# Performance work log

Hardware: AMD Instinct MI355X
Metric: run time of the kernel (lower is better)

Reference implementation:

```python
import jax, jax.numpy as jnp
import numpy as np

WINDOWS = [2, 4, 6]
THR = 0.5


def conv1x1(x, w, b):
    # x: [N,C,H,W], w: [O,C], b: [O]
    return jnp.einsum('nchw,oc->nohw', x, w) + b[None, :, None, None]


def cpool(x):
    # channel max + mean -> [N,2,H,W]
    return jnp.stack([x.max(axis=1), x.mean(axis=1)], axis=1)


def mask_fusion(orin, feature, w1, b1, w2, b2):
    sim = jax.nn.sigmoid(jnp.sum(conv1x1(cpool(orin), w1, b1) * conv1x1(cpool(feature), w2, b2), axis=1, keepdims=True))
    mask = (sim > THR).astype(orin.dtype)
    return mask * feature + (1.0 - mask) * orin


def unfold(x, kh, kw, sh, sw, w):
    # torch F.unfold equivalent -> [N, C*kh*kw, w*w] (channel-major like torch)
    rows = jnp.arange(w)[:, None] * sh + jnp.arange(kh)[None, :]  # [w,kh]
    cols = jnp.arange(w)[:, None] * sw + jnp.arange(kw)[None, :]  # [w,kw]
    p = x[:, :, rows[:, :, None, None], cols[None, None, :, :]]  # [N,C,w,kh,w,kw]
    p = p.transpose(0, 1, 3, 5, 2, 4)  # [N,C,kh,kw,w,w]
    N, C = x.shape[:2]
    return p.reshape(N, C * kh * kw, w * w)


def fold(cols_, H, W, kh, kw, sh, sw, w):
    # torch F.fold equivalent (col2im with overlap-add)
    N, CK, P = cols_.shape
    C = CK // (kh * kw)
    p = cols_.reshape(N, C, kh, kw, w, w).transpose(0, 1, 4, 2, 5, 3).reshape(N, C, w * kh, w * kw)
    r = (jnp.arange(w)[:, None] * sh + jnp.arange(kh)[None, :]).reshape(-1)
    c = (jnp.arange(w)[:, None] * sw + jnp.arange(kw)[None, :]).reshape(-1)
    return jnp.zeros((N, C, H, W), cols_.dtype).at[:, :, r[:, None], c[None, :]].add(p)


def psa(u, wq, wk, wv):
    # u: [N,C,P,L]; scaled dot-product self-attention over L within each patch
    t = u.transpose(0, 2, 3, 1)  # [N,P,L,C]
    q, k, v = t @ wq, t @ wk, t @ wv
    s = jnp.einsum('nplc,npmc->nplm', q, k) / jnp.sqrt(jnp.asarray(t.shape[-1], t.dtype))
    o = jnp.einsum('nplm,npmc->nplc', jax.nn.softmax(s, axis=-1), v)
    return o.transpose(0, 3, 1, 2)


def setup_inputs():
    key = jax.random.key(0)
    ks = jax.random.split(key, 20)
    N, C, H, W = 4, 64, 72, 72
    E = len(WINDOWS) * C
    nrm = lambda k, shape, s: jax.random.normal(k, shape, jnp.float32) * s
    return {
        'x': nrm(ks[0], (N, C, H, W), 1.0),
        'exp_w': nrm(ks[1], (E, C), C ** -0.5), 'exp_b': jnp.zeros((E,), jnp.float32),
        'res_w': nrm(ks[2], (C, E), E ** -0.5), 'res_b': jnp.zeros((C,), jnp.float32),
        'fus_w': nrm(ks[3], (C, C), C ** -0.5), 'fus_b': jnp.zeros((C,), jnp.float32),
        'wq': nrm(ks[4], (C, C), C ** -0.5),
        'wk': nrm(ks[5], (C, C), C ** -0.5),
        'wv': nrm(ks[6], (C, C), C ** -0.5),
        'mf1a_w': nrm(ks[7], (2, 2), 0.7), 'mf1a_b': jnp.zeros((2,), jnp.float32),
        'mf1b_w': nrm(ks[8], (2, 2), 0.7), 'mf1b_b': jnp.zeros((2,), jnp.float32),
        'mf2a_w': nrm(ks[9], (2, 2), 0.7), 'mf2a_b': jnp.zeros((2,), jnp.float32),
        'mf2b_w': nrm(ks[10], (2, 2), 0.7), 'mf2b_b': jnp.zeros((2,), jnp.float32),
    }


def reference(x, exp_w, exp_b, res_w, res_b, fus_w, fus_b, wq, wk, wv,
              mf1a_w, mf1a_b, mf1b_w, mf1b_b, mf2a_w, mf2a_b, mf2b_w, mf2b_b):
    N, C, H, W = x.shape
    expx = conv1x1(x, exp_w, exp_b)  # [N, 3C, H, W]
    parts = jnp.split(expx, len(WINDOWS), axis=1)
    outs = []
    for i, w in enumerate(WINDOWS):
        sh, sw = H // w, W // w
        kh, kw = sh + H % w, sw + W % w
        u = unfold(parts[i], kh, kw, sh, sw, w)       # [N, C*kh*kw, w*w]
        u = u.reshape(N, C, w * w, kh * kw)           # raw reinterpret, as in torch .view
        a = psa(u, wq, wk, wv).reshape(N, C * kh * kw, w * w)
        cnt = fold(jnp.ones_like(a), H, W, kh, kw, sh, sw, w)
        outs.append(fold(a, H, W, kh, kw, sh, sw, w) / cnt)
    out = mask_fusion(jnp.concatenate(outs, axis=1), expx, mf1a_w, mf1a_b, mf1b_w, mf1b_b)
    out = conv1x1(out, res_w, res_b)
    out = mask_fusion(out, x, mf2a_w, mf2a_b, mf2b_w, mf2b_b)
    return conv1x1(out, fus_w, fus_b)
```

## Files before the change

kernel.cpp:

```cpp
#include <hip/hip_runtime.h>

constexpr int CN = 4;
constexpr int CC = 64;
constexpr int CH = 72, CW = 72;
constexpr int HW = CH * CW;
constexpr int NPOS = CN * HW;
constexpr long TOKF = 3L * NPOS * 64;
constexpr long HPAD = 4096;

typedef _Float16 h4 __attribute__((ext_vector_type(4)));
typedef _Float16 h8 __attribute__((ext_vector_type(8)));
typedef float f4 __attribute__((ext_vector_type(4)));

__device__ __forceinline__ int fidx(int row, int g, int off) {
  return (row << 6) + ((g ^ (row & 7)) << 3) + off;
}
__device__ __forceinline__ int f192(int row, int g) {
  return row * 192 + (((g & 24) | ((g ^ row) & 7)) << 3);
}

template <int WW, int SS>
__device__ __forceinline__ void expand_body(const float* __restrict__ x,
                                            const float* __restrict__ w64,
                                            const float* __restrict__ b64,
                                            float* __restrict__ out, int pg) {
  int n = pg / HW;
  int pos = pg - n * HW;
  int h = pos / CW, wcol = pos % CW;

  float xv[64];
  const float* xp = x + (long)n * CC * HW + pos;
#pragma unroll
  for (int c = 0; c < 64; ++c) xv[c] = xp[c * HW];

  int wr = h / SS, kx = h % SS, wcq = wcol / SS, ky = wcol % SS;
  int j = kx * (SS * WW * WW) + ky * (WW * WW) + wr * WW + wcq;
  float* op = out + ((long)n * HW + j) * 64;

#pragma unroll 1
  for (int og = 0; og < 16; ++og) {
    float t0[4];
#pragma unroll
    for (int i = 0; i < 4; ++i) {
      int o = og * 4 + i;
      float acc = b64[o];
      const float* wp = w64 + o * 64;
#pragma unroll
      for (int cg = 0; cg < 16; ++cg) {
        float4 w4 = *(const float4*)(wp + 4 * cg);
        acc = fmaf(xv[4 * cg + 0], w4.x, acc);
        acc = fmaf(xv[4 * cg + 1], w4.y, acc);
        acc = fmaf(xv[4 * cg + 2], w4.z, acc);
        acc = fmaf(xv[4 * cg + 3], w4.w, acc);
      }
      t0[i] = acc;
    }
    *(float4*)(op + og * 4) = make_float4(t0[0], t0[1], t0[2], t0[3]);
  }
}

__global__ __launch_bounds__(256) void k_prep(
    const float* __restrict__ x, const float* __restrict__ exp_w,
    const float* __restrict__ exp_b, const float* __restrict__ wq,
    const float* __restrict__ wk, const float* __restrict__ wv,
    const float* __restrict__ res_w, const float* __restrict__ fus_w,
    float* __restrict__ ex, _Float16* __restrict__ wTh,
    _Float16* __restrict__ wTl, _Float16* __restrict__ rwh,
    _Float16* __restrict__ rwl, _Float16* __restrict__ fwh,
    _Float16* __restrict__ fwl) {
  int b = blockIdx.x;
  if (b >= 243) {
    int i = (b - 243) * 256 + threadIdx.x;
    float v;
    _Float16 *dh, *dl;
    int off;
    if (i < 12288) {
      int m = i >> 12;
      int r = i & 4095;
      int cp = r >> 6, c = r & 63;
      const float* src = (m == 0) ? wq : ((m == 1) ? wk : wv);
      v = src[c * 64 + cp];
      dh = wTh; dl = wTl; off = i;
    } else if (i < 24576) {
      off = i - 12288;
      v = res_w[off];
      dh = rwh; dl = rwl;
    } else {
      off = i - 24576;
      v = fus_w[off];
      dh = fwh; dl = fwl;
    }
    _Float16 h = (_Float16)v;
    dh[off] = h;
    dl[off] = (_Float16)(v - (float)h);
    return;
  }
  int wi = b / 81;
  int pg = (b - wi * 81) * 256 + threadIdx.x;
  if (wi == 0)
    expand_body<2, 36>(x, exp_w, exp_b, ex, pg);
  else if (wi == 1)
    expand_body<4, 18>(x, exp_w + 4096, exp_b + 64, ex + (long)NPOS * 64, pg);
  else
    expand_body<6, 12>(x, exp_w + 8192, exp_b + 128, ex + 2L * NPOS * 64, pg);
}

__global__ __launch_bounds__(256) void k_qkv(
    const float* __restrict__ ex, const _Float16* __restrict__ wTh,
    const _Float16* __restrict__ wTl, _Float16* __restrict__ qh,
    _Float16* __restrict__ ql, _Float16* __restrict__ kh,
    _Float16* __restrict__ kl, _Float16* __restrict__ vth,
    _Float16* __restrict__ vtl) {
  __shared__ __align__(16) _Float16 Wh[12288], Wl[12288];
  __shared__ __align__(16) float Cb[4096];
  _Float16* Eh = (_Float16*)Cb;
  _Float16* El = (_Float16*)Cb + 4096;

  const int tid = threadIdx.x;
  const long tok0 = (long)blockIdx.x * 64;
  const int lane = tid & 63, w = tid >> 6;
  const int lw = lane & 15, lg = lane >> 4;

  {
    int srow = tid >> 2, sfq = tid & 3;
#pragma unroll
    for (int p = 0; p < 4; ++p) {
      int c0 = (4 * p + sfq) * 4;
      float4 v = *(const float4*)(ex + (tok0 + srow) * 64 + c0);
      h4 hh = {(_Float16)v.x, (_Float16)v.y, (_Float16)v.z, (_Float16)v.w};
      h4 ll = {(_Float16)(v.x - (float)hh[0]), (_Float16)(v.y - (float)hh[1]),
               (_Float16)(v.z - (float)hh[2]), (_Float16)(v.w - (float)hh[3])};
      *(h4*)&Eh[fidx(srow, c0 >> 3, c0 & 7)] = hh;
      *(h4*)&El[fidx(srow, c0 >> 3, c0 & 7)] = ll;
    }
  }
#pragma unroll
  for (int it = 0; it < 6; ++it) {
    int idx = it * 256 + tid;
    int row = idx >> 3, gr = idx & 7;
    *(h8*)&Wh[fidx(row, gr, 0)] = *(const h8*)(wTh + idx * 8);
    *(h8*)&Wl[fidx(row, gr, 0)] = *(const h8*)(wTl + idx * 8);
  }
  __syncthreads();

  h8 eh[2], el[2];
#pragma unroll
  for (int s = 0; s < 2; ++s) {
    eh[s] = *(const h8*)&Eh[fidx(w * 16 + lw, s * 4 + lg, 0)];
    el[s] = *(const h8*)&El[fidx(w * 16 + lw, s * 4 + lg, 0)];
  }
  __syncthreads();

  const float SC = 0.125f * 1.4426950408889634f;
#pragma unroll 1
  for (int p = 0; p < 3; ++p) {
#pragma unroll
    for (int ot = 0; ot < 4; ++ot) {
      f4 acc = (f4){0.f, 0.f, 0.f, 0.f};
#pragma unroll
      for (int s = 0; s < 2; ++s) {
        h8 bh = *(const h8*)&Wh[fidx(p * 64 + ot * 16 + lw, s * 4 + lg, 0)];
        h8 bl = *(const h8*)&Wl[fidx(p * 64 + ot * 16 + lw, s * 4 + lg, 0)];
        acc = __builtin_amdgcn_mfma_f32_16x16x32_f16(eh[s], bh, acc, 0, 0, 0);
        acc = __builtin_amdgcn_mfma_f32_16x16x32_f16(el[s], bh, acc, 0, 0, 0);
        acc = __builtin_amdgcn_mfma_f32_16x16x32_f16(eh[s], bl, acc, 0, 0, 0);
      }
#pragma unroll
      for (int r = 0; r < 4; ++r) {
        int row = w * 16 + 4 * lg + r;
        int col = ot * 16 + lw;
        Cb[(row << 6) + ((((col >> 2) ^ (row & 15))) << 2) + (col & 3)] =
            acc[r];
      }
    }
    __syncthreads();

    if (p < 2) {
      int tokl = tid >> 2, off = (tid & 3) * 16;
      float vals[16];
#pragma unroll
      for (int j = 0; j < 4; ++j) {
        int slot = (off >> 2) + j;
        f4 v = *(const f4*)&Cb[(tokl << 6) + (((slot ^ (tokl & 15))) << 2)];
        vals[4 * j + 0] = v[0]; vals[4 * j + 1] = v[1];
        vals[4 * j + 2] = v[2]; vals[4 * j + 3] = v[3];
      }
      float sc = (p == 0) ? SC : 1.0f;
      _Float16* dh = (p == 0 ? qh : kh) + (tok0 + tokl) * 64 + off;
      _Float16* dl = (p == 0 ? ql : kl) + (tok0 + tokl) * 64 + off;
      h8 hh0, hh1, ll0, ll1;
#pragma unroll
      for (int j = 0; j < 8; ++j) {
        float x0 = vals[j] * sc;
        _Float16 h = (_Float16)x0;
        hh0[j] = h;
        ll0[j] = (_Float16)(x0 - (float)h);
        float x1 = vals[8 + j] * sc;
        _Float16 h1 = (_Float16)x1;
        hh1[j] = h1;
        ll1[j] = (_Float16)(x1 - (float)h1);
      }
      *(h8*)dh = hh0; *(h8*)(dh + 8) = hh1;
      *(h8*)dl = ll0; *(h8*)(dl + 8) = ll1;
    } else {
      int ch0 = (tid & 15) * 4, tokl0 = (tid >> 4) * 4;
      float tv[4][4];
#pragma unroll
      for (int r = 0; r < 4; ++r) {
        int row = tokl0 + r;
        int slot = (ch0 >> 2) ^ (row & 15);
        f4 v = *(const f4*)&Cb[(row << 6) + (slot << 2)];
        tv[r][0] = v[0]; tv[r][1] = v[1]; tv[r][2] = v[2]; tv[r][3] = v[3];
      }
      long tokg = tok0 + tokl0;
      int wi = (int)(tokg / NPOS);
      long tl = tokg - (long)wi * NPOS;
      int L = (wi == 0) ? 1296 : ((wi == 1) ? 324 : 144);
      int g = (int)(tl / L);
      int key0 = (int)(tl - (long)g * L);
      long base = (long)wi * NPOS * 64 + (long)g * 64 * L + key0;
#pragma unroll
      for (int i = 0; i < 4; ++i) {
        h4 hh, ll;
#pragma unroll
        for (int r = 0; r < 4; ++r) {
          _Float16 h = (_Float16)tv[r][i];
          hh[r] = h;
          ll[r] = (_Float16)(tv[r][i] - (float)h);
        }
        *(h4*)&vth[base + (long)(ch0 + i) * L] = hh;
        *(h4*)&vtl[base + (long)(ch0 + i) * L] = ll;
      }
    }
    __syncthreads();
  }
}

__global__ __launch_bounds__(256) void k_attn(
    const _Float16* __restrict__ qg, const _Float16* __restrict__ qgl,
    const _Float16* __restrict__ kg, const _Float16* __restrict__ kgl,
    const _Float16* __restrict__ vg, const _Float16* __restrict__ vgl,
    float* __restrict__ og_) {
  __shared__ __align__(16) _Float16 Kh[4096], Kl[4096];
  __shared__ __align__(16) _Float16 Vh[4096], Vl[4096];
  __shared__ __align__(16) _Float16 Ph[4096], Pl[4096];

  const int tid = threadIdx.x;
  int b = blockIdx.x;
  int L, g, qt, NCH;
  long tokbase, vbase;
  if (b < 336) {
    L = 1296; NCH = 21; g = b / 21; qt = b - g * 21;
    tokbase = (long)g * 1296;
    vbase = (long)g * 1296 * 64;
  } else if (b < 720) {
    int t = b - 336;
    L = 324; NCH = 6; g = t / 6; qt = t - g * 6;
    tokbase = (long)NPOS + (long)g * 324;
    vbase = (long)NPOS * 64 + (long)g * 324 * 64;
  } else {
    int t = b - 720;
    L = 144; NCH = 3; g = t / 3; qt = t - g * 3;
    tokbase = 2L * NPOS + (long)g * 144;
    vbase = 2L * NPOS * 64 + (long)g * 144 * 64;
  }

  const int lane = tid & 63, w = tid >> 6;
  const int lw = lane & 15, lg = lane >> 4;
  const int w16 = w * 16;

  h8 qfh[2], qfl[2];
  {
    long qb = (tokbase + (long)qt * 64 + w16 + lw) * 64;
#pragma unroll
    for (int s = 0; s < 2; ++s) {
      qfh[s] = *(const h8*)(qg + qb + (s * 4 + lg) * 8);
      qfl[s] = *(const h8*)(qgl + qb + (s * 4 + lg) * 8);
    }
  }

  float m_s = -1e30f, l_s = 0.f;
  f4 oa[4];
#pragma unroll
  for (int i = 0; i < 4; ++i) oa[i] = (f4){0.f, 0.f, 0.f, 0.f};

  const int krow = tid >> 3, kgr = tid & 7;
  const long ksA = (tokbase + krow) * 64 + kgr * 8;
  const long vsA = vbase + (long)krow * L + kgr * 8;
  const long v32 = (long)32 * L;

  h8 rk0, rk1, rl0, rl1, rv0, rv1, rw0, rw1;
  auto loadKV = [&](int chn) {
    long ko = ksA + ((long)chn << 12);
    long vo = vsA + chn * 64;
    rk0 = *(const h8*)(kg + ko);
    rl0 = *(const h8*)(kgl + ko);
    rv0 = *(const h8*)(vg + vo);
    rw0 = *(const h8*)(vgl + vo);
    rk1 = *(const h8*)(kg + ko + 2048);
    rl1 = *(const h8*)(kgl + ko + 2048);
    rv1 = *(const h8*)(vg + vo + v32);
    rw1 = *(const h8*)(vgl + vo + v32);
  };
  loadKV(0);

  for (int ch = 0; ch < NCH; ++ch) {
    __syncthreads();
    {
      *(h8*)&Kh[fidx(krow, kgr, 0)] = rk0;
      *(h8*)&Kl[fidx(krow, kgr, 0)] = rl0;
      *(h8*)&Vh[fidx(krow, kgr, 0)] = rv0;
      *(h8*)&Vl[fidx(krow, kgr, 0)] = rw0;
      *(h8*)&Kh[fidx(32 + krow, kgr, 0)] = rk1;
      *(h8*)&Kl[fidx(32 + krow, kgr, 0)] = rl1;
      *(h8*)&Vh[fidx(32 + krow, kgr, 0)] = rv1;
      *(h8*)&Vl[fidx(32 + krow, kgr, 0)] = rw1;
    }
    __syncthreads();
    if (ch + 1 < NCH) loadKV(ch + 1);

    f4 sa[4];
#pragma unroll
    for (int kt = 0; kt < 4; ++kt) sa[kt] = (f4){0.f, 0.f, 0.f, 0.f};
#pragma unroll
    for (int slab = 0; slab < 2; ++slab) {
      h8 qbh = qfh[slab];
      h8 qbl = qfl[slab];
#pragma unroll
      for (int kt = 0; kt < 4; ++kt) {
        h8 ah = *(const h8*)&Kh[fidx(kt * 16 + lw, slab * 4 + lg, 0)];
        h8 al = *(const h8*)&Kl[fidx(kt * 16 + lw, slab * 4 + lg, 0)];
        sa[kt] = __builtin_amdgcn_mfma_f32_16x16x32_f16(ah, qbh, sa[kt], 0, 0, 0);
        sa[kt] = __builtin_amdgcn_mfma_f32_16x16x32_f16(al, qbh, sa[kt], 0, 0, 0);
        sa[kt] = __builtin_amdgcn_mfma_f32_16x16x32_f16(ah, qbl, sa[kt], 0, 0, 0);
      }
    }

    float pr[4][4];
    float pmax = -1e30f;
#pragma unroll
    for (int kt = 0; kt < 4; ++kt)
#pragma unroll
      for (int r = 0; r < 4; ++r) {
        int kidx = ch * 64 + kt * 16 + 4 * lg + r;
        float s = (kidx < L) ? sa[kt][r] : -1e30f;
        pr[kt][r] = s;
        pmax = fmaxf(pmax, s);
      }
    pmax = fmaxf(pmax, __shfl_xor(pmax, 16));
    pmax = fmaxf(pmax, __shfl_xor(pmax, 32));
    if (!__all(pmax <= m_s + 8.0f)) {
      float mn = fmaxf(m_s, pmax);
      float fs = exp2f(m_s - mn);
      m_s = mn;
      float fsb[4];
#pragma unroll
      for (int r = 0; r < 4; ++r) fsb[r] = __shfl(fs, 4 * lg + r);
#pragma unroll
      for (int ct = 0; ct < 4; ++ct)
#pragma unroll
        for (int r = 0; r < 4; ++r) oa[ct][r] *= fsb[r];
      l_s *= fs;
    }
    float rs = 0.f;
#pragma unroll
    for (int kt = 0; kt < 4; ++kt)
#pragma unroll
      for (int r = 0; r < 4; ++r) {
        float e = exp2f(pr[kt][r] - m_s);
        pr[kt][r] = e;
        rs += e;
      }
    rs += __shfl_xor(rs, 16);
    rs += __shfl_xor(rs, 32);
    l_s += rs;

#pragma unroll
    for (int kt = 0; kt < 4; ++kt) {
      h4 hh = {(_Float16)pr[kt][0], (_Float16)pr[kt][1], (_Float16)pr[kt][2],
               (_Float16)pr[kt][3]};
      h4 ll = {(_Float16)(pr[kt][0] - (float)hh[0]),
               (_Float16)(pr[kt][1] - (float)hh[1]),
               (_Float16)(pr[kt][2] - (float)hh[2]),
               (_Float16)(pr[kt][3] - (float)hh[3])};
      int key0 = kt * 16 + 4 * lg;
      int kgr2 = key0 >> 3, ko = key0 & 7;
      *(h4*)&Ph[fidx(w16 + lw, kgr2, ko)] = hh;
      *(h4*)&Pl[fidx(w16 + lw, kgr2, ko)] = ll;
    }

#pragma unroll
    for (int slab = 0; slab < 2; ++slab) {
      h8 pah = *(const h8*)&Ph[fidx(w16 + lw, slab * 4 + lg, 0)];
      h8 pal = *(const h8*)&Pl[fidx(w16 + lw, slab * 4 + lg, 0)];
#pragma unroll
      for (int ct = 0; ct < 4; ++ct) {
        h8 vbh = *(const h8*)&Vh[fidx(ct * 16 + lw, slab * 4 + lg, 0)];
        h8 vbl = *(const h8*)&Vl[fidx(ct * 16 + lw, slab * 4 + lg, 0)];
        oa[ct] = __builtin_amdgcn_mfma_f32_16x16x32_f16(pah, vbh, oa[ct], 0, 0, 0);
        oa[ct] = __builtin_amdgcn_mfma_f32_16x16x32_f16(pal, vbh, oa[ct], 0, 0, 0);
        oa[ct] = __builtin_amdgcn_mfma_f32_16x16x32_f16(pah, vbl, oa[ct], 0, 0, 0);
      }
    }
  }

  float linv[4];
#pragma unroll
  for (int r = 0; r < 4; ++r) linv[r] = 1.0f / __shfl(l_s, 4 * lg + r);
#pragma unroll
  for (int r = 0; r < 4; ++r) {
    int qi = qt * 64 + w16 + 4 * lg + r;
    if (qi < L) {
      float* op = og_ + (tokbase + qi) * 64 + lw;
#pragma unroll
      for (int ct = 0; ct < 4; ++ct) op[ct * 16] = oa[ct][r] * linv[r];
    }
  }
}

__global__ __launch_bounds__(256) void k_maskA(
    const float* __restrict__ ex, const float* __restrict__ att,
    const float* __restrict__ m1aw, const float* __restrict__ m1ab,
    const float* __restrict__ m1bw, const float* __restrict__ m1bb,
    _Float16* __restrict__ f1h, _Float16* __restrict__ f1l) {
  const int tid = threadIdx.x;
  const int wv = tid >> 6, lane = tid & 63;
  int pg = blockIdx.x * 4 + wv;
  int n = pg / HW, posn = pg - n * HW;
  int h = posn / CW, wcol = posn % CW;
  auto tok = [&](int S, int W) -> int {
    int wr = h / S, kx = h % S, wcq = wcol / S, ky = wcol % S;
    return kx * (S * W * W) + ky * (W * W) + wr * W + wcq;
  };
  int j0 = tok(36, 2), j1 = tok(18, 4), j2 = tok(12, 6);
  long t0 = ((long)n * HW + j0) * 64 + lane;
  long t1 = ((long)NPOS + (long)n * HW + j1) * 64 + lane;
  long t2 = (2L * NPOS + (long)n * HW + j2) * 64 + lane;
  float av0 = att[t0], av1 = att[t1], av2 = att[t2];
  float ev0 = ex[t0], ev1 = ex[t1], ev2 = ex[t2];
  float mxa = fmaxf(fmaxf(av0, av1), av2), sma = av0 + av1 + av2;
  float mxe = fmaxf(fmaxf(ev0, ev1), ev2), sme = ev0 + ev1 + ev2;
#pragma unroll
  for (int d = 1; d < 64; d <<= 1) {
    mxa = fmaxf(mxa, __shfl_xor(mxa, d));
    sma += __shfl_xor(sma, d);
    mxe = fmaxf(mxe, __shfl_xor(mxe, d));
    sme += __shfl_xor(sme, d);
  }
  float mna = sma * (1.f / 192.f), mne = sme * (1.f / 192.f);
  float ca0 = fmaf(m1aw[0], mxa, fmaf(m1aw[1], mna, m1ab[0]));
  float ca1 = fmaf(m1aw[2], mxa, fmaf(m1aw[3], mna, m1ab[1]));
  float cb0 = fmaf(m1bw[0], mxe, fmaf(m1bw[1], mne, m1bb[0]));
  float cb1 = fmaf(m1bw[2], mxe, fmaf(m1bw[3], mne, m1bb[1]));
  bool mk = (ca0 * cb0 + ca1 * cb1) > 0.f;
  _Float16* fh = f1h + (long)pg * 192 + lane;
  _Float16* fl = f1l + (long)pg * 192 + lane;
  float v0 = mk ? ev0 : av0;
  float v1 = mk ? ev1 : av1;
  float v2 = mk ? ev2 : av2;
  _Float16 h0 = (_Float16)v0, h1 = (_Float16)v1, h2 = (_Float16)v2;
  fh[0] = h0;   fl[0] = (_Float16)(v0 - (float)h0);
  fh[64] = h1;  fl[64] = (_Float16)(v1 - (float)h1);
  fh[128] = h2; fl[128] = (_Float16)(v2 - (float)h2);
}

__global__ __launch_bounds__(256) void k_fuse3(
    const float* __restrict__ x, const _Float16* __restrict__ f1h,
    const _Float16* __restrict__ f1l, const _Float16* __restrict__ rwh,
    const _Float16* __restrict__ rwl, const float* __restrict__ res_b,
    const _Float16* __restrict__ fwh, const _Float16* __restrict__ fwl,
    const float* __restrict__ fus_b, const float* __restrict__ m2aw,
    const float* __restrict__ m2ab, const float* __restrict__ m2bw,
    const float* __restrict__ m2bb, float* __restrict__ out) {
  __shared__ __align__(16) _Float16 F1hS[12288];
  __shared__ __align__(16) _Float16 F1lS[12288];
  float* Cb = (float*)F1hS;
  _Float16* o2h = F1lS;
  _Float16* o2l = F1lS + 4096;

  const int tid = threadIdx.x;
  const int posb = blockIdx.x * 64;
  const int n = posb / HW, posn = posb % HW;
  const int lane = tid & 63, w = tid >> 6;
  const int lw = lane & 15, lg = lane >> 4;
  const int w16 = w * 16;

#pragma unroll
  for (int it = 0; it < 6; ++it) {
    int idx = it * 256 + tid;
    int row = idx / 24, g = idx % 24;
    long src = (long)(posb + row) * 192 + g * 8;
    *(h8*)&F1hS[f192(row, g)] = *(const h8*)(f1h + src);
    *(h8*)&F1lS[f192(row, g)] = *(const h8*)(f1l + src);
  }
  __syncthreads();

  h8 ah[6], al[6];
#pragma unroll
  for (int s = 0; s < 6; ++s) {
    ah[s] = *(const h8*)&F1hS[f192(w16 + lw, s * 4 + lg)];
    al[s] = *(const h8*)&F1lS[f192(w16 + lw, s * 4 + lg)];
  }

  f4 acc[4];
#pragma unroll
  for (int ot = 0; ot < 4; ++ot) {
    float bb = res_b[ot * 16 + lw];
    acc[ot] = (f4){bb, bb, bb, bb};
#pragma unroll
    for (int s = 0; s < 6; ++s) {
      int wo = (ot * 16 + lw) * 192 + (s * 4 + lg) * 8;
      h8 bh = *(const h8*)(rwh + wo);
      h8 bl = *(const h8*)(rwl + wo);
      acc[ot] = __builtin_amdgcn_mfma_f32_16x16x32_f16(ah[s], bh, acc[ot], 0, 0, 0);
      acc[ot] = __builtin_amdgcn_mfma_f32_16x16x32_f16(al[s], bh, acc[ot], 0, 0, 0);
      acc[ot] = __builtin_amdgcn_mfma_f32_16x16x32_f16(ah[s], bl, acc[ot], 0, 0, 0);
    }
  }
  __syncthreads();

#pragma unroll
  for (int ot = 0; ot < 4; ++ot)
#pragma unroll
    for (int r = 0; r < 4; ++r) {
      int row = w16 + 4 * lg + r, col = ot * 16 + lw;
      Cb[(row << 6) + ((((col >> 2) ^ (row & 15))) << 2) + (col & 3)] =
          acc[ot][r];
    }
  __syncthreads();

  const int pos = tid >> 2, off = (tid & 3) * 16;
  float vals[16];
#pragma unroll
  for (int j = 0; j < 4; ++j) {
    int slot = (off >> 2) + j;
    f4 v = *(const f4*)&Cb[(pos << 6) + (((slot ^ (pos & 15))) << 2)];
    vals[4 * j + 0] = v[0]; vals[4 * j + 1] = v[1];
    vals[4 * j + 2] = v[2]; vals[4 * j + 3] = v[3];
  }
  float amx = vals[0], asum = vals[0];
#pragma unroll
  for (int i = 1; i < 16; ++i) {
    amx = fmaxf(amx, vals[i]);
    asum += vals[i];
  }
  amx = fmaxf(amx, __shfl_xor(amx, 1)); asum += __shfl_xor(asum, 1);
  amx = fmaxf(amx, __shfl_xor(amx, 2)); asum += __shfl_xor(asum, 2);
  float xv[16];
  const float* xp = x + ((long)n * CC + off) * HW + posn + pos;
#pragma unroll
  for (int i = 0; i < 16; ++i) xv[i] = xp[i * HW];
  float xmx = xv[0], xsum = xv[0];
#pragma unroll
  for (int i = 1; i < 16; ++i) {
    xmx = fmaxf(xmx, xv[i]);
    xsum += xv[i];
  }
  xmx = fmaxf(xmx, __shfl_xor(xmx, 1)); xsum += __shfl_xor(xsum, 1);
  xmx = fmaxf(xmx, __shfl_xor(xmx, 2)); xsum += __shfl_xor(xsum, 2);
  float rmn = asum * (1.f / 64.f), xmn = xsum * (1.f / 64.f);
  float ca0 = fmaf(m2aw[0], amx, fmaf(m2aw[1], rmn, m2ab[0]));
  float ca1 = fmaf(m2aw[2], amx, fmaf(m2aw[3], rmn, m2ab[1]));
  float cb0 = fmaf(m2bw[0], xmx, fmaf(m2bw[1], xmn, m2bb[0]));
  float cb1 = fmaf(m2bw[2], xmx, fmaf(m2bw[3], xmn, m2bb[1]));
  bool mk2 = (ca0 * cb0 + ca1 * cb1) > 0.f;

#pragma unroll
  for (int hf = 0; hf < 2; ++hf) {
    h8 hh, ll;
#pragma unroll
    for (int j = 0; j < 8; ++j) {
      float v = mk2 ? xv[hf * 8 + j] : vals[hf * 8 + j];
      _Float16 hx = (_Float16)v;
      hh[j] = hx;
      ll[j] = (_Float16)(v - (float)hx);
    }
    int g = (off >> 3) + hf;
    *(h8*)&o2h[fidx(pos, g, 0)] = hh;
    *(h8*)&o2l[fidx(pos, g, 0)] = ll;
  }
  __syncthreads();

  h8 a2h[2], a2l[2];
#pragma unroll
  for (int s = 0; s < 2; ++s) {
    a2h[s] = *(const h8*)&o2h[fidx(w16 + lw, s * 4 + lg, 0)];
    a2l[s] = *(const h8*)&o2l[fidx(w16 + lw, s * 4 + lg, 0)];
  }
  f4 acc2[4];
#pragma unroll
  for (int ot = 0; ot < 4; ++ot) {
    float bb = fus_b[ot * 16 + lw];
    acc2[ot] = (f4){bb, bb, bb, bb};
#pragma unroll
    for (int s = 0; s < 2; ++s) {
      int wo = (ot * 16 + lw) * 64 + (s * 4 + lg) * 8;
      h8 bh = *(const h8*)(fwh + wo);
      h8 bl = *(const h8*)(fwl + wo);
      acc2[ot] = __builtin_amdgcn_mfma_f32_16x16x32_f16(a2h[s], bh, acc2[ot], 0, 0, 0);
      acc2[ot] = __builtin_amdgcn_mfma_f32_16x16x32_f16(a2l[s], bh, acc2[ot], 0, 0, 0);
      acc2[ot] = __builtin_amdgcn_mfma_f32_16x16x32_f16(a2h[s], bl, acc2[ot], 0, 0, 0);
    }
  }
  __syncthreads();

#pragma unroll
  for (int ot = 0; ot < 4; ++ot)
#pragma unroll
    for (int r = 0; r < 4; ++r) {
      int prow = w16 + 4 * lg + r, col = ot * 16 + lw;
      Cb[(prow << 6) + ((col + prow) & 63)] = acc2[ot][r];
    }
  __syncthreads();
#pragma unroll
  for (int i = 0; i < 16; ++i) {
    float v = Cb[(lane << 6) + ((w16 + i + lane) & 63)];
    out[((long)n * CC + w16 + i) * HW + posn + lane] = v;
  }
}

extern "C" void kernel_launch(void* const* d_in, const int* in_sizes, int n_in,
                              void* d_out, int out_size, void* d_ws,
                              size_t ws_size, hipStream_t stream) {
  (void)in_sizes; (void)n_in; (void)out_size;
  const float* x      = (const float*)d_in[0];
  const float* exp_w  = (const float*)d_in[1];
  const float* exp_b  = (const float*)d_in[2];
  const float* res_w  = (const float*)d_in[3];
  const float* res_b  = (const float*)d_in[4];
  const float* fus_w  = (const float*)d_in[5];
  const float* fus_b  = (const float*)d_in[6];
  const float* wq     = (const float*)d_in[7];
  const float* wk     = (const float*)d_in[8];
  const float* wv     = (const float*)d_in[9];
  const float* m1aw   = (const float*)d_in[10];
  const float* m1ab   = (const float*)d_in[11];
  const float* m1bw   = (const float*)d_in[12];
  const float* m1bb   = (const float*)d_in[13];
  const float* m2aw   = (const float*)d_in[14];
  const float* m2ab   = (const float*)d_in[15];
  const float* m2bw   = (const float*)d_in[16];
  const float* m2bb   = (const float*)d_in[17];

  const long HSZ = TOKF + HPAD;
  const size_t needF =
      2 * (size_t)TOKF + (6 * (size_t)HSZ + 2 * 12288 + 2 * 12288 + 2 * 4096) / 2;
  if (ws_size < needF * sizeof(float)) return;
  float* ws = (float*)d_ws;
  float* ex = ws;
  float* ob = ex + TOKF;
  _Float16* qh  = (_Float16*)(ob + TOKF);
  _Float16* ql  = qh + HSZ;
  _Float16* kh  = ql + HSZ;
  _Float16* kl  = kh + HSZ;
  _Float16* vth = kl + HSZ;
  _Float16* vtl = vth + HSZ;
  _Float16* wTh = vtl + HSZ;
  _Float16* wTl = wTh + 12288;
  _Float16* rwh = wTl + 12288;
  _Float16* rwl = rwh + 12288;
  _Float16* fwh = rwl + 12288;
  _Float16* fwl = fwh + 4096;
  _Float16* f1h = qh;
  _Float16* f1l = ql;

  k_prep<<<355, 256, 0, stream>>>(x, exp_w, exp_b, wq, wk, wv, res_w, fus_w,
                                  ex, wTh, wTl, rwh, rwl, fwh, fwl);
  k_qkv<<<972, 256, 0, stream>>>(ex, wTh, wTl, qh, ql, kh, kl, vth, vtl);
  k_attn<<<1152, 256, 0, stream>>>(qh, ql, kh, kl, vth, vtl, ob);
  k_maskA<<<5184, 256, 0, stream>>>(ex, ob, m1aw, m1ab, m1bw, m1bb, f1h, f1l);
  k_fuse3<<<324, 256, 0, stream>>>(x, f1h, f1l, rwh, rwl, res_b, fwh, fwl,
                                   fus_b, m2aw, m2ab, m2bw, m2bb,
                                   (float*)d_out);
}
```

Measured before the change: 153.4 us.

## Fuse first mask-fusion stage into fuse3 kernel and reorder attention block mapping

New measurement: 153.1 us. Within noise of the previous version (-0.2%).

```diff
diff --git a/kernel.cpp b/kernel.cpp
--- a/kernel.cpp
+++ b/kernel.cpp
@@ -250,17 +250,17 @@
   int L, g, qt, NCH;
   long tokbase, vbase;
   if (b < 336) {
-    L = 1296; NCH = 21; g = b / 21; qt = b - g * 21;
+    L = 1296; NCH = 21; g = b & 15; qt = b >> 4;
     tokbase = (long)g * 1296;
     vbase = (long)g * 1296 * 64;
   } else if (b < 720) {
     int t = b - 336;
-    L = 324; NCH = 6; g = t / 6; qt = t - g * 6;
+    L = 324; NCH = 6; g = t & 63; qt = t >> 6;
     tokbase = (long)NPOS + (long)g * 324;
     vbase = (long)NPOS * 64 + (long)g * 324 * 64;
   } else {
     int t = b - 720;
-    L = 144; NCH = 3; g = t / 3; qt = t - g * 3;
+    L = 144; NCH = 3; g = t % 144; qt = t / 144;
     tokbase = 2L * NPOS + (long)g * 144;
     vbase = 2L * NPOS * 64 + (long)g * 144 * 64;
   }
@@ -418,55 +418,11 @@
   }
 }
 
-__global__ __launch_bounds__(256) void k_maskA(
-    const float* __restrict__ ex, const float* __restrict__ att,
-    const float* __restrict__ m1aw, const float* __restrict__ m1ab,
-    const float* __restrict__ m1bw, const float* __restrict__ m1bb,
-    _Float16* __restrict__ f1h, _Float16* __restrict__ f1l) {
-  const int tid = threadIdx.x;
-  const int wv = tid >> 6, lane = tid & 63;
-  int pg = blockIdx.x * 4 + wv;
-  int n = pg / HW, posn = pg - n * HW;
-  int h = posn / CW, wcol = posn % CW;
-  auto tok = [&](int S, int W) -> int {
-    int wr = h / S, kx = h % S, wcq = wcol / S, ky = wcol % S;
-    return kx * (S * W * W) + ky * (W * W) + wr * W + wcq;
-  };
-  int j0 = tok(36, 2), j1 = tok(18, 4), j2 = tok(12, 6);
-  long t0 = ((long)n * HW + j0) * 64 + lane;
-  long t1 = ((long)NPOS + (long)n * HW + j1) * 64 + lane;
-  long t2 = (2L * NPOS + (long)n * HW + j2) * 64 + lane;
-  float av0 = att[t0], av1 = att[t1], av2 = att[t2];
-  float ev0 = ex[t0], ev1 = ex[t1], ev2 = ex[t2];
-  float mxa = fmaxf(fmaxf(av0, av1), av2), sma = av0 + av1 + av2;
-  float mxe = fmaxf(fmaxf(ev0, ev1), ev2), sme = ev0 + ev1 + ev2;
-#pragma unroll
-  for (int d = 1; d < 64; d <<= 1) {
-    mxa = fmaxf(mxa, __shfl_xor(mxa, d));
-    sma += __shfl_xor(sma, d);
-    mxe = fmaxf(mxe, __shfl_xor(mxe, d));
-    sme += __shfl_xor(sme, d);
-  }
-  float mna = sma * (1.f / 192.f), mne = sme * (1.f / 192.f);
-  float ca0 = fmaf(m1aw[0], mxa, fmaf(m1aw[1], mna, m1ab[0]));
-  float ca1 = fmaf(m1aw[2], mxa, fmaf(m1aw[3], mna, m1ab[1]));
-  float cb0 = fmaf(m1bw[0], mxe, fmaf(m1bw[1], mne, m1bb[0]));
-  float cb1 = fmaf(m1bw[2], mxe, fmaf(m1bw[3], mne, m1bb[1]));
-  bool mk = (ca0 * cb0 + ca1 * cb1) > 0.f;
-  _Float16* fh = f1h + (long)pg * 192 + lane;
-  _Float16* fl = f1l + (long)pg * 192 + lane;
-  float v0 = mk ? ev0 : av0;
-  float v1 = mk ? ev1 : av1;
-  float v2 = mk ? ev2 : av2;
-  _Float16 h0 = (_Float16)v0, h1 = (_Float16)v1, h2 = (_Float16)v2;
-  fh[0] = h0;   fl[0] = (_Float16)(v0 - (float)h0);
-  fh[64] = h1;  fl[64] = (_Float16)(v1 - (float)h1);
-  fh[128] = h2; fl[128] = (_Float16)(v2 - (float)h2);
-}
-
 __global__ __launch_bounds__(256) void k_fuse3(
-    const float* __restrict__ x, const _Float16* __restrict__ f1h,
-    const _Float16* __restrict__ f1l, const _Float16* __restrict__ rwh,
+    const float* __restrict__ x, const float* __restrict__ ex,
+    const float* __restrict__ att, const float* __restrict__ m1aw,
+    const float* __restrict__ m1ab, const float* __restrict__ m1bw,
+    const float* __restrict__ m1bb, const _Float16* __restrict__ rwh,
     const _Float16* __restrict__ rwl, const float* __restrict__ res_b,
     const _Float16* __restrict__ fwh, const _Float16* __restrict__ fwl,
     const float* __restrict__ fus_b, const float* __restrict__ m2aw,
@@ -485,13 +441,53 @@
   const int lw = lane & 15, lg = lane >> 4;
   const int w16 = w * 16;
 
-#pragma unroll
-  for (int it = 0; it < 6; ++it) {
-    int idx = it * 256 + tid;
-    int row = idx / 24, g = idx % 24;
-    long src = (long)(posb + row) * 192 + g * 8;
-    *(h8*)&F1hS[f192(row, g)] = *(const h8*)(f1h + src);
-    *(h8*)&F1lS[f192(row, g)] = *(const h8*)(f1l + src);
+  {
+    float w1a0 = m1aw[0], w1a1 = m1aw[1], w1a2 = m1aw[2], w1a3 = m1aw[3];
+    float b1a0 = m1ab[0], b1a1 = m1ab[1];
+    float w1b0 = m1bw[0], w1b1 = m1bw[1], w1b2 = m1bw[2], w1b3 = m1bw[3];
+    float b1b0 = m1bb[0], b1b1 = m1bb[1];
+#pragma unroll 1
+    for (int pp = 0; pp < 16; ++pp) {
+      int pl = w * 16 + pp;
+      int pos = posn + pl;
+      int h = pos / CW, wcol = pos % CW;
+      auto tok = [&](int S, int W) -> int {
+        int wr = h / S, kx = h % S, wcq = wcol / S, ky = wcol % S;
+        return kx * (S * W * W) + ky * (W * W) + wr * W + wcq;
+      };
+      int j0 = tok(36, 2), j1 = tok(18, 4), j2 = tok(12, 6);
+      long t0 = ((long)n * HW + j0) * 64 + lane;
+      long t1 = ((long)NPOS + (long)n * HW + j1) * 64 + lane;
+      long t2 = (2L * NPOS + (long)n * HW + j2) * 64 + lane;
+      float av0 = att[t0], av1 = att[t1], av2 = att[t2];
+      float ev0 = ex[t0], ev1 = ex[t1], ev2 = ex[t2];
+      float mxa = fmaxf(fmaxf(av0, av1), av2), sma = av0 + av1 + av2;
+      float mxe = fmaxf(fmaxf(ev0, ev1), ev2), sme = ev0 + ev1 + ev2;
+#pragma unroll
+      for (int d = 1; d < 64; d <<= 1) {
+        mxa = fmaxf(mxa, __shfl_xor(mxa, d));
+        sma += __shfl_xor(sma, d);
+        mxe = fmaxf(mxe, __shfl_xor(mxe, d));
+        sme += __shfl_xor(sme, d);
+      }
+      float mna = sma * (1.f / 192.f), mne = sme * (1.f / 192.f);
+      float ca0 = fmaf(w1a0, mxa, fmaf(w1a1, mna, b1a0));
+      float ca1 = fmaf(w1a2, mxa, fmaf(w1a3, mna, b1a1));
+      float cb0 = fmaf(w1b0, mxe, fmaf(w1b1, mne, b1b0));
+      float cb1 = fmaf(w1b2, mxe, fmaf(w1b3, mne, b1b1));
+      bool mk = (ca0 * cb0 + ca1 * cb1) > 0.f;
+      float v0 = mk ? ev0 : av0;
+      float v1 = mk ? ev1 : av1;
+      float v2 = mk ? ev2 : av2;
+      _Float16 h0 = (_Float16)v0, h1 = (_Float16)v1, h2 = (_Float16)v2;
+      int c0 = lane, c1 = lane + 64, c2 = lane + 128;
+      F1hS[f192(pl, c0 >> 3) + (c0 & 7)] = h0;
+      F1lS[f192(pl, c0 >> 3) + (c0 & 7)] = (_Float16)(v0 - (float)h0);
+      F1hS[f192(pl, c1 >> 3) + (c1 & 7)] = h1;
+      F1lS[f192(pl, c1 >> 3) + (c1 & 7)] = (_Float16)(v1 - (float)h1);
+      F1hS[f192(pl, c2 >> 3) + (c2 & 7)] = h2;
+      F1lS[f192(pl, c2 >> 3) + (c2 & 7)] = (_Float16)(v2 - (float)h2);
+    }
   }
   __syncthreads();
 
@@ -661,15 +657,12 @@
   _Float16* rwl = rwh + 12288;
   _Float16* fwh = rwl + 12288;
   _Float16* fwl = fwh + 4096;
-  _Float16* f1h = qh;
-  _Float16* f1l = ql;
 
   k_prep<<<355, 256, 0, stream>>>(x, exp_w, exp_b, wq, wk, wv, res_w, fus_w,
                                   ex, wTh, wTl, rwh, rwl, fwh, fwl);
   k_qkv<<<972, 256, 0, stream>>>(ex, wTh, wTl, qh, ql, kh, kl, vth, vtl);
   k_attn<<<1152, 256, 0, stream>>>(qh, ql, kh, kl, vth, vtl, ob);
-  k_maskA<<<5184, 256, 0, stream>>>(ex, ob, m1aw, m1ab, m1bw, m1bb, f1h, f1l);
-  k_fuse3<<<324, 256, 0, stream>>>(x, f1h, f1l, rwh, rwl, res_b, fwh, fwl,
-                                   fus_b, m2aw, m2ab, m2bw, m2bb,
-                                   (float*)d_out);
-}
+  k_fuse3<<<324, 256, 0, stream>>>(x, ex, ob, m1aw, m1ab, m1bw, m1bb, rwh,
+                                   rwl, res_b, fwh, fwl, fus_b, m2aw, m2ab,
+                                   m2bw, m2bb, (float*)d_out);
+}
```
